# Optimization experiments

Measured on AMD Instinct MI355X. Metric: run time of the kernel, lower is better.

## Reference

```python
import jax, jax.numpy as jnp
import numpy as np

BATCH = 8192
IN_DIM = 2048
OUT_DIM = 2048
DEPTH = 5


def setup_inputs() -> dict:
    key = jax.random.key(0)
    k1, k2, k3, k4 = jax.random.split(key, 4)
    x = jax.random.normal(k1, (BATCH, IN_DIM), dtype=jnp.float32)
    hyperdimensional_weights = jax.random.normal(k2, (DEPTH, IN_DIM, OUT_DIM), dtype=jnp.float32)
    classical_weights = jax.random.normal(k3, (IN_DIM, OUT_DIM), dtype=jnp.float32)
    classical_biases = jax.random.normal(k4, (OUT_DIM,), dtype=jnp.float32)
    return {
        "x": x,
        "hyperdimensional_weights": hyperdimensional_weights,
        "classical_weights": classical_weights,
        "classical_biases": classical_biases,
    }


def _hyperdimensional_probs(hd_w):
    # angle = W[d, j, 0], phase = W[d, j, 1] for output index j (j < input_dims)
    depth, in_dim, _ = hd_w.shape
    angles = hd_w[:, :OUT_DIM, 0]   # [depth, out]
    phases = hd_w[:, :OUT_DIM, 1]   # [depth, out]
    # Initial uniform state 1/sqrt(n), replicated per output unit j.
    s0 = jnp.full((OUT_DIM, in_dim), 1.0 / np.sqrt(in_dim), dtype=jnp.complex64)

    def step(s, ang_ph):
        ang, ph = ang_ph                      # each [out]
        c = jnp.cos(ang)[:, None]
        sn = jnp.sin(ang)[:, None]
        # Circulant rotation: new[k] = cos*s[k] - sin*s[k+1] + sin*s[k-1] (cyclic)
        s = c * s - sn * jnp.roll(s, -1, axis=1) + sn * jnp.roll(s, 1, axis=1)
        # Global phase gate: diag(e^{i*phase})
        s = s * jnp.exp(1j * ph)[:, None]
        return s, None

    s, _ = jax.lax.scan(step, s0, (angles, phases))
    # probability = |state[0]|^2
    return jnp.abs(s[:, 0]) ** 2              # [out], real float32


def reference(x, hyperdimensional_weights, classical_weights, classical_biases):
    classical = x @ classical_weights + classical_biases            # [B, out]
    hd = _hyperdimensional_probs(hyperdimensional_weights)          # [out] (batch-independent)
    return jnp.tanh(classical + hd[None, :])
```

## Files before the change

### kernel.cpp

```cpp
#include <hip/hip_runtime.h>

#define BATCH 8192
#define DIM   2048
#define DEPTH 5

#define TM 128
#define TN 128
#define BK 32
#define KDIM 2048

typedef short bf16x8_t __attribute__((ext_vector_type(8)));
typedef float f32x4_t  __attribute__((ext_vector_type(4)));

__device__ __forceinline__ unsigned short f2bf(float f) {
  unsigned u = __float_as_uint(f);
  u += 0x7fffu + ((u >> 16) & 1u);
  return (unsigned short)(u >> 16);
}
__device__ __forceinline__ float bf2f(unsigned short h) {
  return __uint_as_float(((unsigned)h) << 16);
}

__global__ void prep_bias_kernel(const float* __restrict__ hdw,
                                 const float* __restrict__ bias,
                                 float* __restrict__ bias2) {
  int j = blockIdx.x * 256 + threadIdx.x;
  float p = 1.0f;
#pragma unroll
  for (int d = 0; d < DEPTH; ++d) {
    p *= cosf(hdw[(size_t)d * DIM * DIM + (size_t)j * DIM]);
  }
  bias2[j] = bias[j] + p * p * (1.0f / 2048.0f);
}

__global__ void split_x_kernel(const float4* __restrict__ x,
                               ushort4* __restrict__ xhi,
                               ushort4* __restrict__ xlo) {
  size_t i = (size_t)blockIdx.x * 256 + threadIdx.x;
  float4 v = x[i];
  ushort4 h, l;
  h.x = f2bf(v.x); l.x = f2bf(v.x - bf2f(h.x));
  h.y = f2bf(v.y); l.y = f2bf(v.y - bf2f(h.y));
  h.z = f2bf(v.z); l.z = f2bf(v.z - bf2f(h.z));
  h.w = f2bf(v.w); l.w = f2bf(v.w - bf2f(h.w));
  xhi[i] = h;
  xlo[i] = l;
}

__global__ void split_wT_kernel(const float* __restrict__ W,
                                unsigned short* __restrict__ whi,
                                unsigned short* __restrict__ wlo) {
  __shared__ float tile[32][33];
  const int tx = threadIdx.x;
  const int ty = threadIdx.y;
  const int n0 = blockIdx.x * 32;
  const int k0 = blockIdx.y * 32;
#pragma unroll
  for (int r = 0; r < 32; r += 8)
    tile[ty + r][tx] = W[(size_t)(k0 + ty + r) * DIM + n0 + tx];
  __syncthreads();
#pragma unroll
  for (int r = 0; r < 32; r += 8) {
    float v = tile[tx][ty + r];
    unsigned short h = f2bf(v);
    unsigned short l = f2bf(v - bf2f(h));
    size_t o = (size_t)(n0 + ty + r) * DIM + k0 + tx;
    whi[o] = h;
    wlo[o] = l;
  }
}

__device__ __forceinline__ void stage_tile(const unsigned short* gbase,
                                           unsigned short* s, int wave, int lane) {
#pragma unroll
  for (int r = 0; r < 2; ++r) {
    int slot = r * 256 + wave * 64 + lane;
    const unsigned short* gp = gbase + (slot >> 2) * KDIM + (slot & 3) * 8;
    unsigned short* lp = s + (r * 256 + wave * 64) * 8;
    __builtin_amdgcn_global_load_lds(
        (const __attribute__((address_space(1))) void*)gp,
        (__attribute__((address_space(3))) void*)lp, 16, 0, 0);
  }
}

__global__ __launch_bounds__(256) void gemm_x3_kernel(
    const unsigned short* __restrict__ Ahi, const unsigned short* __restrict__ Alo,
    const unsigned short* __restrict__ Bhi, const unsigned short* __restrict__ Blo,
    const float* __restrict__ bias2, float* __restrict__ out) {
  __shared__ __attribute__((aligned(16))) unsigned short sAhi[TM * BK];
  __shared__ __attribute__((aligned(16))) unsigned short sAlo[TM * BK];
  __shared__ __attribute__((aligned(16))) unsigned short sBhi[TN * BK];
  __shared__ __attribute__((aligned(16))) unsigned short sBlo[TN * BK];

  const int tid  = threadIdx.x;
  const int wave = tid >> 6;
  const int lane = tid & 63;
  const int bm = blockIdx.x;
  const int bn = blockIdx.y;
  const int wm = wave >> 1, wn = wave & 1;
  const int l15 = lane & 15, kl = lane >> 4;

  const unsigned short* agh = Ahi + (size_t)bm * TM * KDIM;
  const unsigned short* agl = Alo + (size_t)bm * TM * KDIM;
  const unsigned short* bgh = Bhi + (size_t)bn * TN * KDIM;
  const unsigned short* bgl = Blo + (size_t)bn * TN * KDIM;

  int aidx[4], bidx[4];
#pragma unroll
  for (int i = 0; i < 4; ++i) {
    aidx[i] = (wm * 64 + i * 16 + l15) * BK + kl * 8;
    bidx[i] = (wn * 64 + i * 16 + l15) * BK + kl * 8;
  }

  const f32x4_t vzero = {0.f, 0.f, 0.f, 0.f};
  f32x4_t acc[4][4];
#pragma unroll
  for (int i = 0; i < 4; ++i)
#pragma unroll
    for (int j = 0; j < 4; ++j) acc[i][j] = vzero;

  for (int kt = 0; kt < KDIM / BK; ++kt) {
    if (kt) __syncthreads();
    const int ko = kt * BK;
    stage_tile(agh + ko, sAhi, wave, lane);
    stage_tile(agl + ko, sAlo, wave, lane);
    stage_tile(bgh + ko, sBhi, wave, lane);
    stage_tile(bgl + ko, sBlo, wave, lane);
    asm volatile("s_waitcnt vmcnt(0)" ::: "memory");
    __syncthreads();

    bf16x8_t ah[4], al[4], bh[4], bl[4];
#pragma unroll
    for (int i = 0; i < 4; ++i) {
      ah[i] = *(const bf16x8_t*)(sAhi + aidx[i]);
      al[i] = *(const bf16x8_t*)(sAlo + aidx[i]);
      bh[i] = *(const bf16x8_t*)(sBhi + bidx[i]);
      bl[i] = *(const bf16x8_t*)(sBlo + bidx[i]);
    }
#pragma unroll
    for (int i = 0; i < 4; ++i)
#pragma unroll
      for (int j = 0; j < 4; ++j) {
        acc[i][j] = __builtin_amdgcn_mfma_f32_16x16x32_bf16(ah[i], bh[j], acc[i][j], 0, 0, 0);
        acc[i][j] = __builtin_amdgcn_mfma_f32_16x16x32_bf16(ah[i], bl[j], acc[i][j], 0, 0, 0);
        acc[i][j] = __builtin_amdgcn_mfma_f32_16x16x32_bf16(al[i], bh[j], acc[i][j], 0, 0, 0);
      }
  }

  const int orow0 = bm * TM + wm * 64;
  const int ocol0 = bn * TN + wn * 64;
#pragma unroll
  for (int j = 0; j < 4; ++j) {
    const int col = ocol0 + j * 16 + l15;
    const float b2 = bias2[col];
#pragma unroll
    for (int i = 0; i < 4; ++i) {
      const int row = orow0 + i * 16 + kl * 4;
#pragma unroll
      for (int r = 0; r < 4; ++r) {
        float z = acc[i][j][r] + b2;
        float e = __expf(2.0f * z);
        out[(size_t)(row + r) * DIM + col] = 1.0f - 2.0f / (e + 1.0f);
      }
    }
  }
}

extern "C" void kernel_launch(void* const* d_in, const int* in_sizes, int n_in,
                              void* d_out, int out_size, void* d_ws, size_t ws_size,
                              hipStream_t stream) {
  const float* x   = (const float*)d_in[0];
  const float* hdw = (const float*)d_in[1];
  const float* W   = (const float*)d_in[2];
  const float* b   = (const float*)d_in[3];
  float* out = (float*)d_out;

  char* ws = (char*)d_ws;
  float*          bias2 = (float*)ws;
  unsigned short* xhi   = (unsigned short*)(ws + 8192);
  unsigned short* xlo   = xhi + (size_t)BATCH * DIM;
  unsigned short* wThi  = xlo + (size_t)BATCH * DIM;
  unsigned short* wTlo  = wThi + (size_t)DIM * DIM;

  prep_bias_kernel<<<DIM / 256, 256, 0, stream>>>(hdw, b, bias2);
  split_x_kernel<<<(BATCH * DIM / 4) / 256, 256, 0, stream>>>(
      (const float4*)x, (ushort4*)xhi, (ushort4*)xlo);
  split_wT_kernel<<<dim3(DIM / 32, DIM / 32), dim3(32, 8), 0, stream>>>(W, wThi, wTlo);
  gemm_x3_kernel<<<dim3(BATCH / TM, DIM / TN), 256, 0, stream>>>(
      xhi, xlo, wThi, wTlo, bias2, out);
}
```

Before: 406.9 us.

## Fuse prep kernels and use conflict-free fragment-major LDS layout for GEMM tiles

Merges the bias, x-split and W-transpose-split kernels into one launch that dispatches work by block index, removing two kernel launches. Changes the global-to-LDS staging so each 16-row by 32-k fragment is stored contiguously in the order lanes consume it. Each lane's MFMA operand read then becomes a contiguous 16-byte access at lane*8, which is meant to remove LDS bank conflicts. The global load pattern changes to 16 rows per wave instruction, which may slightly alter coalescing.

```diff
diff --git a/kernel.cpp b/kernel.cpp
--- a/kernel.cpp
+++ b/kernel.cpp
@@ -21,52 +21,55 @@
   return __uint_as_float(((unsigned)h) << 16);
 }
 
-__global__ void prep_bias_kernel(const float* __restrict__ hdw,
-                                 const float* __restrict__ bias,
-                                 float* __restrict__ bias2) {
-  int j = blockIdx.x * 256 + threadIdx.x;
-  float p = 1.0f;
+__global__ void prep_fused_kernel(const float* __restrict__ x,
+                                  const float* __restrict__ hdw,
+                                  const float* __restrict__ W,
+                                  const float* __restrict__ bias,
+                                  float* __restrict__ bias2,
+                                  ushort4* __restrict__ xhi4,
+                                  ushort4* __restrict__ xlo4,
+                                  unsigned short* __restrict__ whi,
+                                  unsigned short* __restrict__ wlo) {
+  __shared__ float tile[32][33];
+  const int b = blockIdx.x;
+  const int tid = threadIdx.x;
+
+  if (b < 16384) {
+    size_t i = (size_t)b * 256 + tid;
+    float4 v = ((const float4*)x)[i];
+    ushort4 h, l;
+    h.x = f2bf(v.x); l.x = f2bf(v.x - bf2f(h.x));
+    h.y = f2bf(v.y); l.y = f2bf(v.y - bf2f(h.y));
+    h.z = f2bf(v.z); l.z = f2bf(v.z - bf2f(h.z));
+    h.w = f2bf(v.w); l.w = f2bf(v.w - bf2f(h.w));
+    xhi4[i] = h;
+    xlo4[i] = l;
+  } else if (b < 20480) {
+    const int t = b - 16384;
+    const int tx = tid & 31;
+    const int ty = tid >> 5;
+    const int n0 = (t & 63) * 32;
+    const int k0 = (t >> 6) * 32;
 #pragma unroll
-  for (int d = 0; d < DEPTH; ++d) {
-    p *= cosf(hdw[(size_t)d * DIM * DIM + (size_t)j * DIM]);
-  }
-  bias2[j] = bias[j] + p * p * (1.0f / 2048.0f);
-}
-
-__global__ void split_x_kernel(const float4* __restrict__ x,
-                               ushort4* __restrict__ xhi,
-                               ushort4* __restrict__ xlo) {
-  size_t i = (size_t)blockIdx.x * 256 + threadIdx.x;
-  float4 v = x[i];
-  ushort4 h, l;
-  h.x = f2bf(v.x); l.x = f2bf(v.x - bf2f(h.x));
-  h.y = f2bf(v.y); l.y = f2bf(v.y - bf2f(h.y));
-  h.z = f2bf(v.z); l.z = f2bf(v.z - bf2f(h.z));
-  h.w = f2bf(v.w); l.w = f2bf(v.w - bf2f(h.w));
-  xhi[i] = h;
-  xlo[i] = l;
-}
-
-__global__ void split_wT_kernel(const float* __restrict__ W,
-                                unsigned short* __restrict__ whi,
-                                unsigned short* __restrict__ wlo) {
-  __shared__ float tile[32][33];
-  const int tx = threadIdx.x;
-  const int ty = threadIdx.y;
-  const int n0 = blockIdx.x * 32;
-  const int k0 = blockIdx.y * 32;
+    for (int r = 0; r < 32; r += 8)
+      tile[ty + r][tx] = W[(size_t)(k0 + ty + r) * DIM + n0 + tx];
+    __syncthreads();
 #pragma unroll
-  for (int r = 0; r < 32; r += 8)
-    tile[ty + r][tx] = W[(size_t)(k0 + ty + r) * DIM + n0 + tx];
-  __syncthreads();
+    for (int r = 0; r < 32; r += 8) {
+      float v = tile[tx][ty + r];
+      unsigned short h = f2bf(v);
+      unsigned short l = f2bf(v - bf2f(h));
+      size_t o = (size_t)(n0 + ty + r) * DIM + k0 + tx;
+      whi[o] = h;
+      wlo[o] = l;
+    }
+  } else {
+    int j = (b - 20480) * 256 + tid;
+    float p = 1.0f;
 #pragma unroll
-  for (int r = 0; r < 32; r += 8) {
-    float v = tile[tx][ty + r];
-    unsigned short h = f2bf(v);
-    unsigned short l = f2bf(v - bf2f(h));
-    size_t o = (size_t)(n0 + ty + r) * DIM + k0 + tx;
-    whi[o] = h;
-    wlo[o] = l;
+    for (int d = 0; d < DEPTH; ++d)
+      p *= cosf(hdw[(size_t)d * DIM * DIM + (size_t)j * DIM]);
+    bias2[j] = bias[j] + p * p * (1.0f / 2048.0f);
   }
 }
 
@@ -74,8 +77,9 @@
                                            unsigned short* s, int wave, int lane) {
 #pragma unroll
   for (int r = 0; r < 2; ++r) {
-    int slot = r * 256 + wave * 64 + lane;
-    const unsigned short* gp = gbase + (slot >> 2) * KDIM + (slot & 3) * 8;
+    const int rg = r * 4 + wave;
+    const unsigned short* gp =
+        gbase + (size_t)(rg * 16 + (lane & 15)) * KDIM + (lane >> 4) * 8;
     unsigned short* lp = s + (r * 256 + wave * 64) * 8;
     __builtin_amdgcn_global_load_lds(
         (const __attribute__((address_space(1))) void*)gp,
@@ -108,8 +112,8 @@
   int aidx[4], bidx[4];
 #pragma unroll
   for (int i = 0; i < 4; ++i) {
-    aidx[i] = (wm * 64 + i * 16 + l15) * BK + kl * 8;
-    bidx[i] = (wn * 64 + i * 16 + l15) * BK + kl * 8;
+    aidx[i] = (wm * 4 + i) * 512 + lane * 8;
+    bidx[i] = (wn * 4 + i) * 512 + lane * 8;
   }
 
   const f32x4_t vzero = {0.f, 0.f, 0.f, 0.f};
@@ -182,10 +186,8 @@
   unsigned short* wThi  = xlo + (size_t)BATCH * DIM;
   unsigned short* wTlo  = wThi + (size_t)DIM * DIM;
 
-  prep_bias_kernel<<<DIM / 256, 256, 0, stream>>>(hdw, b, bias2);
-  split_x_kernel<<<(BATCH * DIM / 4) / 256, 256, 0, stream>>>(
-      (const float4*)x, (ushort4*)xhi, (ushort4*)xlo);
-  split_wT_kernel<<<dim3(DIM / 32, DIM / 32), dim3(32, 8), 0, stream>>>(W, wThi, wTlo);
+  prep_fused_kernel<<<20488, 256, 0, stream>>>(
+      x, hdw, W, b, bias2, (ushort4*)xhi, (ushort4*)xlo, wThi, wTlo);
   gemm_x3_kernel<<<dim3(BATCH / TM, DIM / TN), 256, 0, stream>>>(
       xhi, xlo, wThi, wTlo, bias2, out);
 }
```

Result: slower. 441.5 us (+8.5%).
